# Optimization experiments

Hardware: AMD Instinct MI355X
Metric: run time of the kernel (lower is better)

## Reference

```python
import jax, jax.numpy as jnp
import numpy as np

N_NODES = 50000
IN_F = 128
OUT_F = 128
N_EDGES = 800000
N_TRAIN = 5000


def setup_inputs() -> dict:
    key = jax.random.key(0)
    ks = jax.random.split(key, 7)
    x = jax.random.normal(ks[0], (N_NODES, IN_F), dtype=jnp.float32)
    edge_rows = jax.random.randint(ks[1], (N_EDGES,), 0, N_NODES)
    edge_cols = jax.random.randint(ks[2], (N_EDGES,), 0, N_NODES)
    adj_vals = jax.random.uniform(ks[3], (N_EDGES,), dtype=jnp.float32)
    train_fts_id = jax.random.randint(ks[4], (N_TRAIN,), 0, N_NODES)
    # xavier_uniform with gain sqrt(2)
    lim_W = np.sqrt(2.0) * np.sqrt(6.0 / (IN_F + OUT_F))
    W = jax.random.uniform(ks[5], (IN_F, OUT_F), dtype=jnp.float32, minval=-lim_W, maxval=lim_W)
    lim_M = np.sqrt(2.0) * np.sqrt(6.0 / (N_NODES + IN_F))
    M = jax.random.uniform(ks[6], (N_NODES, IN_F), dtype=jnp.float32, minval=-lim_M, maxval=lim_M)
    return {"x": x, "edge_rows": edge_rows, "edge_cols": edge_cols,
            "adj_vals": adj_vals, "train_fts_id": train_fts_id, "M": M, "W": W}


def reference(x, edge_rows, edge_cols, adj_vals, train_fts_id, M, W):
    n_nodes = M.shape[0]
    # M_eff = sigmoid(M), with rows at train_fts_id fixed to 1.0
    train_mask = jnp.zeros((n_nodes, 1), dtype=M.dtype).at[train_fts_id].set(1.0)
    M_eff = jnp.where(train_mask > 0, 1.0, jax.nn.sigmoid(M))  # [N, F]
    # AM = (non_norm_adj @ M_eff)^-1, inf -> 0 (binary non-normalized adjacency)
    denom = jax.ops.segment_sum(M_eff[edge_cols], edge_rows, num_segments=n_nodes)  # [N, F]
    AM = jnp.where(denom == 0, 0.0, 1.0 / jnp.where(denom == 0, 1.0, denom))
    # H = (sp_adj @ (M_eff * x)) * AM
    msg = adj_vals[:, None] * (M_eff * x)[edge_cols]  # [E, F]
    H = jax.ops.segment_sum(msg, edge_rows, num_segments=n_nodes) * AM  # [N, F]
    return jax.nn.elu(H @ W)  # [N, OUT_F]
```

## Files before the change

### kernel.cpp

```cpp
#include <hip/hip_runtime.h>
#include <hip/hip_fp16.h>

#define NN 50000
#define FF 128
#define NE 800000
#define NT 5000
#define NF (NN * FF)
#define NBKT 196
#define BCAP 8192
#define PADCOL 50000u

typedef __attribute__((ext_vector_type(8))) short bf16x8;
typedef __attribute__((ext_vector_type(4))) float f32x4;
typedef __attribute__((ext_vector_type(4))) unsigned u32x4;
typedef __attribute__((ext_vector_type(2))) unsigned u32x2;
typedef __attribute__((ext_vector_type(4))) int i32x4;

__device__ __forceinline__ unsigned bf16_rne(float f) {
    unsigned u = __float_as_uint(f);
    return (u + 0x7FFFu + ((u >> 16) & 1u)) >> 16;
}

__global__ void k_init(int* __restrict__ gcur, int* __restrict__ flags) {
    int i = blockIdx.x * blockDim.x + threadIdx.x;
    if (i < 256) gcur[i] = 0;
    if (i < NN) flags[i] = 0;
}

__global__ void k_flags(const int* __restrict__ ids, int* __restrict__ flags) {
    int i = blockIdx.x * blockDim.x + threadIdx.x;
    if (i < NT) flags[ids[i]] = 1;
}

__global__ void k_pack(const float* __restrict__ M, const float* __restrict__ x,
                       const int* __restrict__ flags, unsigned* __restrict__ Q) {
    int i4 = blockIdx.x * blockDim.x + threadIdx.x;
    if (i4 >= NF / 4 + FF / 4) return;
    u32x4* Q4 = reinterpret_cast<u32x4*>(Q);
    if (i4 >= NF / 4) {
        u32x4 z = {0, 0, 0, 0};
        Q4[i4] = z;
        return;
    }
    int node = (i4 * 4) >> 7;
    int trn = flags[node];
    f32x4 m = __builtin_nontemporal_load(reinterpret_cast<const f32x4*>(M) + i4);
    f32x4 xv = __builtin_nontemporal_load(reinterpret_cast<const f32x4*>(x) + i4);
    float me0 = trn ? 1.0f : 1.0f / (1.0f + __expf(-m.x));
    float me1 = trn ? 1.0f : 1.0f / (1.0f + __expf(-m.y));
    float me2 = trn ? 1.0f : 1.0f / (1.0f + __expf(-m.z));
    float me3 = trn ? 1.0f : 1.0f / (1.0f + __expf(-m.w));
    u32x4 q;
    q.x = bf16_rne(me0) | (bf16_rne(me0 * xv.x) << 16);
    q.y = bf16_rne(me1) | (bf16_rne(me1 * xv.y) << 16);
    q.z = bf16_rne(me2) | (bf16_rne(me2 * xv.z) << 16);
    q.w = bf16_rne(me3) | (bf16_rne(me3 * xv.w) << 16);
    Q4[i4] = q;
}

__global__ __launch_bounds__(1024)
void k_pass1(const int* __restrict__ rows, const int* __restrict__ cols,
             const float* __restrict__ adj, int* __restrict__ gcur,
             unsigned long long* __restrict__ ebuf) {
    __shared__ int hist[256];
    __shared__ int cur[256];
    int t = threadIdx.x;
    if (t < 256) hist[t] = 0;
    __syncthreads();
    int base = blockIdx.x * 8192;
    int r[8], c[8], bkt[8];
    float a[8];
#pragma unroll
    for (int k = 0; k < 8; ++k) {
        int idx = base + k * 1024 + t;
        bool v = idx < NE;
        r[k] = v ? rows[idx] : 0;
        c[k] = v ? cols[idx] : 0;
        a[k] = v ? adj[idx] : 0.f;
        bkt[k] = v ? (r[k] >> 8) : -1;
        if (v) atomicAdd(&hist[bkt[k]], 1);
    }
    __syncthreads();
    if (t < 256) {
        int cnt = hist[t];
        int b = 0;
        if (cnt > 0) b = atomicAdd(&gcur[t], cnt);
        cur[t] = b;
    }
    __syncthreads();
#pragma unroll
    for (int k = 0; k < 8; ++k) {
        if (bkt[k] >= 0) {
            int p = atomicAdd(&cur[bkt[k]], 1);
            if (p < BCAP) {
                unsigned h = (unsigned)__half_as_ushort(__float2half_rn(a[k]));
                unsigned pk = (unsigned)c[k] | (h << 16);
                ebuf[(size_t)bkt[k] * BCAP + p] =
                    ((unsigned long long)(r[k] & 255) << 32) | pk;
            }
        }
    }
}

__global__ void k_scanb(const int* __restrict__ gcur, int* __restrict__ gbase) {
    __shared__ int part[256];
    int t = threadIdx.x;
    int own = min(gcur[t], BCAP);
    part[t] = own;
    __syncthreads();
    for (int d = 1; d < 256; d <<= 1) {
        int v = (t >= d) ? part[t - d] : 0;
        __syncthreads();
        part[t] += v;
        __syncthreads();
    }
    gbase[t] = part[t] - own;
}

__global__ __launch_bounds__(1024)
void k_pass2(const int* __restrict__ gcur, const int* __restrict__ gbase,
             const unsigned long long* __restrict__ ebuf,
             unsigned* __restrict__ gedges, int* __restrict__ offsets) {
    __shared__ int hist[256];
    __shared__ int scan[256];
    __shared__ int cur[256];
    int b = blockIdx.x;
    int t = threadIdx.x;
    int cnt = min(gcur[b], BCAP);
    int gstart = gbase[b];
    if (t < 256) hist[t] = 0;
    __syncthreads();
    const unsigned long long* eb = ebuf + (size_t)b * BCAP;
    unsigned long long rec[8];
    int nk = (cnt + 1023) >> 10;
    for (int k = 0; k < nk; ++k) {
        int idx = k * 1024 + t;
        rec[k] = 0;
        if (idx < cnt) {
            rec[k] = eb[idx];
            atomicAdd(&hist[(int)(rec[k] >> 32)], 1);
        }
    }
    __syncthreads();
    if (t < 256) scan[t] = hist[t];
    __syncthreads();
    for (int d = 1; d < 256; d <<= 1) {
        int v = (t < 256 && t >= d) ? scan[t - d] : 0;
        __syncthreads();
        if (t < 256) scan[t] += v;
        __syncthreads();
    }
    if (t < 256) {
        int excl = scan[t] - hist[t];
        cur[t] = excl;
        int row = b * 256 + t;
        if (row < NN) offsets[row] = gstart + excl;
    }
    if (b == NBKT - 1 && t == 0) offsets[NN] = gstart + cnt;
    __syncthreads();
    for (int k = 0; k < nk; ++k) {
        int idx = k * 1024 + t;
        if (idx < cnt) {
            int lr = (int)(rec[k] >> 32);
            int p = atomicAdd(&cur[lr], 1);
            gedges[gstart + p] = (unsigned)(rec[k] & 0xFFFFFFFFu);
        }
    }
}

__global__ __launch_bounds__(256)
void k_gather(const int* __restrict__ offsets, const unsigned* __restrict__ gedges,
              const unsigned* __restrict__ Q, unsigned* __restrict__ Hnb) {
    int t = blockIdx.x * blockDim.x + threadIdx.x;
    int wv = t >> 6;
    int lane = t & 63;
    int ra = wv * 2, rb = ra + 1;
    if (ra >= NN) return;
    int ba = offsets[ra];
    int bb = offsets[rb];
    int eb2 = offsets[rb + 1];
    int dega = bb - ba, degb = eb2 - bb;
    int nmax = (max(dega, degb) + 3) >> 2;
    const u32x2* Q2 = reinterpret_cast<const u32x2*>(Q);
    const unsigned padrec = PADCOL;
    float da0 = 0.f, da1 = 0.f, ha0 = 0.f, ha1 = 0.f;
    float db0 = 0.f, db1 = 0.f, hb0 = 0.f, hb1 = 0.f;
    for (int c = 0; c < nmax; ++c) {
        int ia = ba + c * 4, ib = bb + c * 4;
        unsigned ea[4], ebv[4];
#pragma unroll
        for (int i = 0; i < 4; ++i) {
            ea[i]  = (ia + i < bb)  ? gedges[ia + i] : padrec;
            ebv[i] = (ib + i < eb2) ? gedges[ib + i] : padrec;
        }
#pragma unroll
        for (int i = 0; i < 4; ++i) {
            unsigned ca = ea[i] & 0xFFFFu, cb = ebv[i] & 0xFFFFu;
            float aa = __half2float(__ushort_as_half((unsigned short)(ea[i] >> 16)));
            float ab = __half2float(__ushort_as_half((unsigned short)(ebv[i] >> 16)));
            u32x2 qa = Q2[(int)ca * 64 + lane];
            u32x2 qb = Q2[(int)cb * 64 + lane];
            da0 += __uint_as_float(qa.x << 16);
            da1 += __uint_as_float(qa.y << 16);
            ha0 += aa * __uint_as_float(qa.x & 0xFFFF0000u);
            ha1 += aa * __uint_as_float(qa.y & 0xFFFF0000u);
            db0 += __uint_as_float(qb.x << 16);
            db1 += __uint_as_float(qb.y << 16);
            hb0 += ab * __uint_as_float(qb.x & 0xFFFF0000u);
            hb1 += ab * __uint_as_float(qb.y & 0xFFFF0000u);
        }
    }
    float oa0 = (da0 == 0.f) ? 0.f : ha0 / da0;
    float oa1 = (da1 == 0.f) ? 0.f : ha1 / da1;
    float ob0 = (db0 == 0.f) ? 0.f : hb0 / db0;
    float ob1 = (db1 == 0.f) ? 0.f : hb1 / db1;
    Hnb[ra * 64 + lane] = bf16_rne(oa0) | (bf16_rne(oa1) << 16);
    Hnb[rb * 64 + lane] = bf16_rne(ob0) | (bf16_rne(ob1) << 16);
}

__global__ __launch_bounds__(256)
void k_gemm(const unsigned* __restrict__ Hnb, const float* __restrict__ W,
            float* __restrict__ out) {
    __shared__ short Wb[128 * 128];
    int tid = threadIdx.x;

#pragma unroll
    for (int i = 0; i < 8; ++i) {
        int c = tid + i * 256;
        int nl = c & 15;
        int t8 = (c >> 4) & 7;
        int ks = (c >> 7) & 3;
        int lh = (c >> 9) & 3;
        int l = nl | (lh << 4);
        int n = t8 * 16 + nl;
        int k0 = ks * 32 + lh * 8;
        short v[8];
#pragma unroll
        for (int j = 0; j < 8; ++j)
            v[j] = (short)bf16_rne(W[(k0 + j) * 128 + n]);
        *reinterpret_cast<bf16x8*>(&Wb[((t8 * 4 + ks) * 64 + l) * 8]) =
            *reinterpret_cast<bf16x8*>(v);
    }
    __syncthreads();

    int wave = tid >> 6, lane = tid & 63;
    int r0 = blockIdx.x * 64 + wave * 16;
    int mrow = lane & 15;
    int kg = lane >> 4;
    int arow = min(r0 + mrow, NN - 1);
    const u32x4* H4 = reinterpret_cast<const u32x4*>(Hnb);

    bf16x8 a[4];
#pragma unroll
    for (int ks = 0; ks < 4; ++ks) {
        u32x4 v = H4[(size_t)arow * 16 + ks * 4 + kg];
        a[ks] = *reinterpret_cast<bf16x8*>(&v);
    }

    f32x4 acc[8];
#pragma unroll
    for (int t8 = 0; t8 < 8; ++t8) acc[t8] = (f32x4){0.f, 0.f, 0.f, 0.f};

#pragma unroll
    for (int t8 = 0; t8 < 8; ++t8) {
#pragma unroll
        for (int ks = 0; ks < 4; ++ks) {
            bf16x8 b = *reinterpret_cast<const bf16x8*>(
                &Wb[((t8 * 4 + ks) * 64 + lane) * 8]);
            acc[t8] = __builtin_amdgcn_mfma_f32_16x16x32_bf16(a[ks], b, acc[t8], 0, 0, 0);
        }
    }

    int colb = lane & 15;
    int rsub = (lane >> 4) * 4;
#pragma unroll
    for (int t8 = 0; t8 < 8; ++t8) {
#pragma unroll
        for (int rg = 0; rg < 4; ++rg) {
            int row = r0 + rsub + rg;
            if (row < NN) {
                float v = acc[t8][rg];
                float o = (v > 0.f) ? v : (__expf(v) - 1.0f);
                __builtin_nontemporal_store(o, &out[(size_t)row * 128 + t8 * 16 + colb]);
            }
        }
    }
}

__global__ void k_init_fb(float* __restrict__ denomH, int* __restrict__ flags) {
    int i = blockIdx.x * blockDim.x + threadIdx.x;
    const int total4 = (2 * NF) / 4;
    if (i < total4)
        reinterpret_cast<float4*>(denomH)[i] = make_float4(0.f, 0.f, 0.f, 0.f);
    if (i < NN) flags[i] = 0;
}

__global__ __launch_bounds__(256)
void k_edge_fb(const int* __restrict__ rows, const int* __restrict__ cols,
               const float* __restrict__ adj, const float* __restrict__ M,
               const int* __restrict__ flags, const float* __restrict__ x,
               float* __restrict__ denom, float* __restrict__ H) {
    int t = blockIdx.x * blockDim.x + threadIdx.x;
    int e = t >> 6;
    int lane = t & 63;
    if (e >= NE) return;
    int r = rows[e], c = cols[e];
    float a = adj[e];
#pragma unroll
    for (int i = 0; i < 2; ++i) {
        int f = lane + i * 64;
        float m = M[c * FF + f];
        float me = flags[c] ? 1.0f : 1.0f / (1.0f + __expf(-m));
        float xv = x[c * FF + f];
        unsafeAtomicAdd(&denom[r * FF + f], me);
        unsafeAtomicAdd(&H[r * FF + f], a * me * xv);
    }
}

__global__ __launch_bounds__(256)
void k_norm_fb(const float* __restrict__ H, const float* __restrict__ denom,
               float* __restrict__ Hn) {
    int i = blockIdx.x * blockDim.x + threadIdx.x;
    if (i >= NF) return;
    float d = denom[i];
    Hn[i] = (d == 0.f) ? 0.f : H[i] / d;
}

__global__ __launch_bounds__(256)
void k_gemm_fb(const float* __restrict__ Hn, const float* __restrict__ W,
               float* __restrict__ out) {
    __shared__ float Ws[128][128];
    __shared__ float Hs[32][128];
    int tid = threadIdx.x;
    const float4* W4 = reinterpret_cast<const float4*>(W);
    float4* Ws4 = reinterpret_cast<float4*>(&Ws[0][0]);
#pragma unroll
    for (int i = 0; i < 16; ++i) Ws4[tid + i * 256] = W4[tid + i * 256];
    int r0 = blockIdx.x * 32;
    const float4* H4 = reinterpret_cast<const float4*>(Hn);
    float4* Hs4 = reinterpret_cast<float4*>(&Hs[0][0]);
#pragma unroll
    for (int i = 0; i < 4; ++i) {
        int m = tid + i * 256;
        int r = m >> 5, k4 = m & 31;
        int row = r0 + r;
        Hs4[m] = (row < NN) ? H4[row * 32 + k4] : make_float4(0.f, 0.f, 0.f, 0.f);
    }
    __syncthreads();
    int c = tid & 127, rg = tid >> 7;
    float acc[16];
#pragma unroll
    for (int i = 0; i < 16; ++i) acc[i] = 0.f;
    for (int k = 0; k < 128; k += 4) {
        float w0 = Ws[k][c], w1 = Ws[k + 1][c], w2 = Ws[k + 2][c], w3 = Ws[k + 3][c];
#pragma unroll
        for (int i = 0; i < 16; ++i) {
            float4 h = *reinterpret_cast<const float4*>(&Hs[rg * 16 + i][k]);
            acc[i] += h.x * w0 + h.y * w1 + h.z * w2 + h.w * w3;
        }
    }
#pragma unroll
    for (int i = 0; i < 16; ++i) {
        int row = r0 + rg * 16 + i;
        if (row < NN) {
            float v = acc[i];
            out[row * 128 + c] = (v > 0.f) ? v : (__expf(v) - 1.0f);
        }
    }
}

extern "C" void kernel_launch(void* const* d_in, const int* in_sizes, int n_in,
                              void* d_out, int out_size, void* d_ws, size_t ws_size,
                              hipStream_t stream) {
    const float* x     = (const float*)d_in[0];
    const int*   erows = (const int*)d_in[1];
    const int*   ecols = (const int*)d_in[2];
    const float* adj   = (const float*)d_in[3];
    const int*   train = (const int*)d_in[4];
    const float* M     = (const float*)d_in[5];
    const float* W     = (const float*)d_in[6];
    float* out = (float*)d_out;
    float* ws  = (float*)d_ws;

    const size_t UNI = ((size_t)NBKT * BCAP * 2 > (size_t)NF / 2)
                           ? (size_t)NBKT * BCAP * 2 : (size_t)NF / 2;
    size_t fo = 0;
    unsigned* Q   = (unsigned*)(ws + fo); fo += NF + FF;
    unsigned* Hnb = (unsigned*)(ws + fo);
    unsigned long long* ebuf = (unsigned long long*)(ws + fo); fo += UNI;
    unsigned* gedges = (unsigned*)(ws + fo); fo += NE;
    int* offsets  = (int*)(ws + fo); fo += NN + 1;
    int* gcur     = (int*)(ws + fo); fo += 256;
    int* gbase    = (int*)(ws + fo); fo += 256;
    int* flags    = (int*)(ws + fo); fo += NN;
    const size_t need = fo * 4;

    if (ws_size >= need) {
        k_init<<<(NN + 255) / 256, 256, 0, stream>>>(gcur, flags);
        k_flags<<<(NT + 255) / 256, 256, 0, stream>>>(train, flags);
        k_pack<<<(NF / 4 + FF / 4 + 255) / 256, 256, 0, stream>>>(M, x, flags, Q);
        k_pass1<<<(NE + 8191) / 8192, 1024, 0, stream>>>(erows, ecols, adj, gcur, ebuf);
        k_scanb<<<1, 256, 0, stream>>>(gcur, gbase);
        k_pass2<<<NBKT, 1024, 0, stream>>>(gcur, gbase, ebuf, gedges, offsets);
        k_gather<<<((NN / 2) * 64 + 255) / 256, 256, 0, stream>>>(offsets, gedges, Q, Hnb);
        k_gemm<<<(NN + 63) / 64, 256, 0, stream>>>(Hnb, W, out);
    } else {
        float* denom = ws;
        float* H     = ws + NF;
        int* flags_fb = (int*)(ws + 2 * (size_t)NF);
        k_init_fb<<<(2 * NF / 4 + 255) / 256, 256, 0, stream>>>(denom, flags_fb);
        k_flags<<<(NT + 255) / 256, 256, 0, stream>>>(train, flags_fb);
        k_edge_fb<<<((size_t)NE * 64 + 255) / 256, 256, 0, stream>>>(
            erows, ecols, adj, M, flags_fb, x, denom, H);
        k_norm_fb<<<(NF + 255) / 256, 256, 0, stream>>>(H, denom, denom);
        k_gemm_fb<<<(NN + 31) / 32, 256, 0, stream>>>(denom, W, out);
    }
}
```

Measured before the change: 115.6 us.

## Fold init, flags and bucket-scan kernels into pack, pass1 and pass2

Drops the separate init, flags and bucket-scan kernels. Train rows are no longer looked up through a flags array. Instead, extra blocks in pass1 overwrite those rows of Q with M_eff=1 after pack has written sigmoid values. The gcur reset moves into pack, and every pass2 block recomputes the 196-bucket prefix scan redundantly. This cuts the launch count from eight to five and removes the flags traffic, in exchange for repeated scan work and an ordering dependence between pack and pass1 on Q.

```diff
diff --git a/kernel.cpp b/kernel.cpp
--- a/kernel.cpp
+++ b/kernel.cpp
@@ -9,6 +9,8 @@
 #define NBKT 196
 #define BCAP 8192
 #define PADCOL 50000u
+#define P1BLK 98
+#define TRN_THREADS (NT * 32)
 
 typedef __attribute__((ext_vector_type(8))) short bf16x8;
 typedef __attribute__((ext_vector_type(4))) float f32x4;
@@ -21,20 +23,10 @@
     return (u + 0x7FFFu + ((u >> 16) & 1u)) >> 16;
 }
 
-__global__ void k_init(int* __restrict__ gcur, int* __restrict__ flags) {
-    int i = blockIdx.x * blockDim.x + threadIdx.x;
-    if (i < 256) gcur[i] = 0;
-    if (i < NN) flags[i] = 0;
-}
-
-__global__ void k_flags(const int* __restrict__ ids, int* __restrict__ flags) {
-    int i = blockIdx.x * blockDim.x + threadIdx.x;
-    if (i < NT) flags[ids[i]] = 1;
-}
-
 __global__ void k_pack(const float* __restrict__ M, const float* __restrict__ x,
-                       const int* __restrict__ flags, unsigned* __restrict__ Q) {
+                       unsigned* __restrict__ Q, int* __restrict__ gcur) {
     int i4 = blockIdx.x * blockDim.x + threadIdx.x;
+    if (i4 < 256) gcur[i4] = 0;
     if (i4 >= NF / 4 + FF / 4) return;
     u32x4* Q4 = reinterpret_cast<u32x4*>(Q);
     if (i4 >= NF / 4) {
@@ -42,14 +34,12 @@
         Q4[i4] = z;
         return;
     }
-    int node = (i4 * 4) >> 7;
-    int trn = flags[node];
     f32x4 m = __builtin_nontemporal_load(reinterpret_cast<const f32x4*>(M) + i4);
     f32x4 xv = __builtin_nontemporal_load(reinterpret_cast<const f32x4*>(x) + i4);
-    float me0 = trn ? 1.0f : 1.0f / (1.0f + __expf(-m.x));
-    float me1 = trn ? 1.0f : 1.0f / (1.0f + __expf(-m.y));
-    float me2 = trn ? 1.0f : 1.0f / (1.0f + __expf(-m.z));
-    float me3 = trn ? 1.0f : 1.0f / (1.0f + __expf(-m.w));
+    float me0 = 1.0f / (1.0f + __expf(-m.x));
+    float me1 = 1.0f / (1.0f + __expf(-m.y));
+    float me2 = 1.0f / (1.0f + __expf(-m.z));
+    float me3 = 1.0f / (1.0f + __expf(-m.w));
     u32x4 q;
     q.x = bf16_rne(me0) | (bf16_rne(me0 * xv.x) << 16);
     q.y = bf16_rne(me1) | (bf16_rne(me1 * xv.y) << 16);
@@ -60,11 +50,28 @@
 
 __global__ __launch_bounds__(1024)
 void k_pass1(const int* __restrict__ rows, const int* __restrict__ cols,
-             const float* __restrict__ adj, int* __restrict__ gcur,
-             unsigned long long* __restrict__ ebuf) {
+             const float* __restrict__ adj, const int* __restrict__ train,
+             const float* __restrict__ x, unsigned* __restrict__ Q,
+             int* __restrict__ gcur, unsigned long long* __restrict__ ebuf) {
+    int t = threadIdx.x;
+    if (blockIdx.x >= P1BLK) {
+        int g = (blockIdx.x - P1BLK) * 1024 + t;
+        if (g < TRN_THREADS) {
+            int ti = g >> 5;
+            int f4 = g & 31;
+            int id = train[ti];
+            f32x4 xv = reinterpret_cast<const f32x4*>(x)[id * 32 + f4];
+            u32x4 q;
+            q.x = 0x3F80u | (bf16_rne(xv.x) << 16);
+            q.y = 0x3F80u | (bf16_rne(xv.y) << 16);
+            q.z = 0x3F80u | (bf16_rne(xv.z) << 16);
+            q.w = 0x3F80u | (bf16_rne(xv.w) << 16);
+            reinterpret_cast<u32x4*>(Q)[id * 32 + f4] = q;
+        }
+        return;
+    }
     __shared__ int hist[256];
     __shared__ int cur[256];
-    int t = threadIdx.x;
     if (t < 256) hist[t] = 0;
     __syncthreads();
     int base = blockIdx.x * 8192;
@@ -102,41 +109,37 @@
     }
 }
 
-__global__ void k_scanb(const int* __restrict__ gcur, int* __restrict__ gbase) {
-    __shared__ int part[256];
-    int t = threadIdx.x;
-    int own = min(gcur[t], BCAP);
-    part[t] = own;
-    __syncthreads();
-    for (int d = 1; d < 256; d <<= 1) {
-        int v = (t >= d) ? part[t - d] : 0;
-        __syncthreads();
-        part[t] += v;
-        __syncthreads();
-    }
-    gbase[t] = part[t] - own;
-}
-
 __global__ __launch_bounds__(1024)
-void k_pass2(const int* __restrict__ gcur, const int* __restrict__ gbase,
+void k_pass2(const int* __restrict__ gcur,
              const unsigned long long* __restrict__ ebuf,
              unsigned* __restrict__ gedges, int* __restrict__ offsets) {
     __shared__ int hist[256];
     __shared__ int scan[256];
     __shared__ int cur[256];
+    __shared__ int bscan[256];
     int b = blockIdx.x;
     int t = threadIdx.x;
+    if (t < 256) {
+        bscan[t] = (t < NBKT) ? min(gcur[t], BCAP) : 0;
+        hist[t] = 0;
+    }
+    __syncthreads();
+    for (int d = 1; d < 256; d <<= 1) {
+        int v = (t < 256 && t >= d) ? bscan[t - d] : 0;
+        __syncthreads();
+        if (t < 256) bscan[t] += v;
+        __syncthreads();
+    }
     int cnt = min(gcur[b], BCAP);
-    int gstart = gbase[b];
-    if (t < 256) hist[t] = 0;
-    __syncthreads();
+    int gstart = (b > 0) ? bscan[b - 1] : 0;
     const unsigned long long* eb = ebuf + (size_t)b * BCAP;
     unsigned long long rec[8];
-    int nk = (cnt + 1023) >> 10;
-    for (int k = 0; k < nk; ++k) {
+#pragma unroll
+    for (int k = 0; k < 8; ++k) {
         int idx = k * 1024 + t;
         rec[k] = 0;
-        if (idx < cnt) {
+        bool v = idx < cnt;
+        if (v) {
             rec[k] = eb[idx];
             atomicAdd(&hist[(int)(rec[k] >> 32)], 1);
         }
@@ -158,7 +161,8 @@
     }
     if (b == NBKT - 1 && t == 0) offsets[NN] = gstart + cnt;
     __syncthreads();
-    for (int k = 0; k < nk; ++k) {
+#pragma unroll
+    for (int k = 0; k < 8; ++k) {
         int idx = k * 1024 + t;
         if (idx < cnt) {
             int lr = (int)(rec[k] >> 32);
@@ -295,6 +299,11 @@
     if (i < NN) flags[i] = 0;
 }
 
+__global__ void k_flags_fb(const int* __restrict__ ids, int* __restrict__ flags) {
+    int i = blockIdx.x * blockDim.x + threadIdx.x;
+    if (i < NT) flags[ids[i]] = 1;
+}
+
 __global__ __launch_bounds__(256)
 void k_edge_fb(const int* __restrict__ rows, const int* __restrict__ cols,
                const float* __restrict__ adj, const float* __restrict__ M,
@@ -391,17 +400,14 @@
     unsigned* gedges = (unsigned*)(ws + fo); fo += NE;
     int* offsets  = (int*)(ws + fo); fo += NN + 1;
     int* gcur     = (int*)(ws + fo); fo += 256;
-    int* gbase    = (int*)(ws + fo); fo += 256;
-    int* flags    = (int*)(ws + fo); fo += NN;
     const size_t need = fo * 4;
 
     if (ws_size >= need) {
-        k_init<<<(NN + 255) / 256, 256, 0, stream>>>(gcur, flags);
-        k_flags<<<(NT + 255) / 256, 256, 0, stream>>>(train, flags);
-        k_pack<<<(NF / 4 + FF / 4 + 255) / 256, 256, 0, stream>>>(M, x, flags, Q);
-        k_pass1<<<(NE + 8191) / 8192, 1024, 0, stream>>>(erows, ecols, adj, gcur, ebuf);
-        k_scanb<<<1, 256, 0, stream>>>(gcur, gbase);
-        k_pass2<<<NBKT, 1024, 0, stream>>>(gcur, gbase, ebuf, gedges, offsets);
+        const int trn_blocks = (TRN_THREADS + 1023) / 1024;
+        k_pack<<<(NF / 4 + FF / 4 + 255) / 256, 256, 0, stream>>>(M, x, Q, gcur);
+        k_pass1<<<P1BLK + trn_blocks, 1024, 0, stream>>>(
+            erows, ecols, adj, train, x, Q, gcur, ebuf);
+        k_pass2<<<NBKT, 1024, 0, stream>>>(gcur, ebuf, gedges, offsets);
         k_gather<<<((NN / 2) * 64 + 255) / 256, 256, 0, stream>>>(offsets, gedges, Q, Hnb);
         k_gemm<<<(NN + 63) / 64, 256, 0, stream>>>(Hnb, W, out);
     } else {
@@ -409,7 +415,7 @@
         float* H     = ws + NF;
         int* flags_fb = (int*)(ws + 2 * (size_t)NF);
         k_init_fb<<<(2 * NF / 4 + 255) / 256, 256, 0, stream>>>(denom, flags_fb);
-        k_flags<<<(NT + 255) / 256, 256, 0, stream>>>(train, flags_fb);
+        k_flags_fb<<<(NT + 255) / 256, 256, 0, stream>>>(train, flags_fb);
         k_edge_fb<<<((size_t)NE * 64 + 255) / 256, 256, 0, stream>>>(
             erows, ecols, adj, M, flags_fb, x, denom, H);
         k_norm_fb<<<(NF + 255) / 256, 256, 0, stream>>>(H, denom, denom);
```

Measured after the change: 107.3 us. 7.2% less time.
